# Optimization experiments

Measured on AMD Instinct MI355X. Metric: run time of the kernel, lower is better.

Reference implementation:

```python
import jax, jax.numpy as jnp
import numpy as np

B, S, D = 4, 2048, 1024
E = 8           # num_experts
TOP_K = 2
H = 3 * D       # hidden_mult = 3


def setup_inputs() -> dict:
    key = jax.random.key(0)
    ks = jax.random.split(key, 5)
    scale_d = 1.0 / np.sqrt(D)
    scale_h = 1.0 / np.sqrt(H)
    return {
        "x": jax.random.normal(ks[0], (B, S, D), dtype=jnp.float32),
        "gate_w": jax.random.normal(ks[1], (D, E), dtype=jnp.float32) * scale_d,
        "w1": jax.random.normal(ks[2], (E, D, H), dtype=jnp.float32) * scale_d,
        "w3": jax.random.normal(ks[3], (E, D, H), dtype=jnp.float32) * scale_d,
        "w2": jax.random.normal(ks[4], (E, H, D), dtype=jnp.float32) * scale_h,
    }


def reference(x, gate_w, w1, w2, w3):
    b, s, d = x.shape
    t = b * s
    xf = x.reshape(t, d)                                  # [T, D]
    probs = jax.nn.softmax(xf @ gate_w, axis=-1)          # [T, E]
    vals, idx = jax.lax.top_k(probs, TOP_K)               # [T, K]
    w = vals / jnp.sum(vals, axis=-1, keepdims=True)      # renormalized top-k weights
    # per-token combine weight for each expert (scatter top-k weights)
    comb = jnp.zeros((t, E), dtype=x.dtype).at[
        jnp.arange(t)[:, None], idx
    ].add(w)                                              # [T, E]
    out = jnp.zeros_like(xf)
    for e in range(E):  # small fixed expert count
        h = jax.nn.silu(xf @ w1[e]) * (xf @ w3[e])        # [T, H] SwiGLU
        out = out + comb[:, e:e + 1] * (h @ w2[e])        # weighted combine
    return out.reshape(b, s, d)
```

## Files before the change

### kernel.cpp

```cpp
#include <hip/hip_runtime.h>
#include <stdint.h>

#define T_TOK 8192
#define DDIM 1024
#define NEXP 8
#define HDIM 3072

typedef __attribute__((ext_vector_type(8))) short bfrag;
typedef __attribute__((ext_vector_type(4))) float facc;

__device__ __forceinline__ void gload16(const void* g, void* l) {
  __builtin_amdgcn_global_load_lds(
      (const __attribute__((address_space(1))) void*)g,
      (__attribute__((address_space(3))) void*)l, 16, 0, 0);
}

__device__ __forceinline__ unsigned short f2bf(float f) {
  unsigned int u = __float_as_uint(f);
  u += 0x7FFFu + ((u >> 16) & 1u);
  return (unsigned short)(u >> 16);
}

__global__ __launch_bounds__(64) void gate_topk(
    const float* __restrict__ x, const float* __restrict__ gw,
    int* __restrict__ counts, int* __restrict__ tok_list,
    float* __restrict__ wt_list)
{
  const int t = blockIdx.x;
  const int lane = threadIdx.x;
  const float* xr = x + (size_t)t * DDIM;
  float p[NEXP];
#pragma unroll
  for (int e = 0; e < NEXP; ++e) p[e] = 0.f;
#pragma unroll 4
  for (int i = 0; i < DDIM / 64; ++i) {
    const int d = i * 64 + lane;
    const float xv = xr[d];
    const float4 g0 = *(const float4*)(gw + (size_t)d * NEXP);
    const float4 g1 = *(const float4*)(gw + (size_t)d * NEXP + 4);
    p[0] += xv * g0.x; p[1] += xv * g0.y; p[2] += xv * g0.z; p[3] += xv * g0.w;
    p[4] += xv * g1.x; p[5] += xv * g1.y; p[6] += xv * g1.z; p[7] += xv * g1.w;
  }
#pragma unroll
  for (int off = 32; off > 0; off >>= 1) {
#pragma unroll
    for (int e = 0; e < NEXP; ++e) p[e] += __shfl_down(p[e], off);
  }
  if (lane == 0) {
    int i1 = 0; float v1 = p[0];
#pragma unroll
    for (int e = 1; e < NEXP; ++e) if (p[e] > v1) { v1 = p[e]; i1 = e; }
    int i2 = -1; float v2 = -3.4e38f;
#pragma unroll
    for (int e = 0; e < NEXP; ++e) if (e != i1 && p[e] > v2) { v2 = p[e]; i2 = e; }
    const float w0 = 1.f / (1.f + __expf(v2 - v1));
    int q1 = atomicAdd(&counts[i1 * 32], 1);
    tok_list[i1 * T_TOK + q1] = t;
    wt_list[i1 * T_TOK + q1] = w0;
    int q2 = atomicAdd(&counts[i2 * 32], 1);
    tok_list[i2 * T_TOK + q2] = t;
    wt_list[i2 * T_TOK + q2] = 1.f - w0;
  }
}

__global__ void calc_offs(const int* __restrict__ counts, int* __restrict__ offs) {
  if (threadIdx.x == 0 && blockIdx.x == 0) {
    int a = 0;
#pragma unroll
    for (int e = 0; e < NEXP; ++e) { offs[e] = a; a += counts[e * 32]; }
    offs[NEXP] = a;
  }
}

__global__ __launch_bounds__(256) void convert_x(
    const float* __restrict__ x, unsigned short* __restrict__ xb)
{
  const size_t i8 = ((size_t)blockIdx.x * 256 + threadIdx.x) * 8;
  const float4 a = *(const float4*)(x + i8);
  const float4 b = *(const float4*)(x + i8 + 4);
  union { unsigned short s[8]; uint4 v; } t;
  t.s[0] = f2bf(a.x); t.s[1] = f2bf(a.y); t.s[2] = f2bf(a.z); t.s[3] = f2bf(a.w);
  t.s[4] = f2bf(b.x); t.s[5] = f2bf(b.y); t.s[6] = f2bf(b.z); t.s[7] = f2bf(b.w);
  *(uint4*)(xb + i8) = t.v;
}

__global__ __launch_bounds__(256) void convert_wT(
    const float* __restrict__ src, unsigned short* __restrict__ dst,
    int K, int N)
{
  const int e = blockIdx.z;
  const int k0 = blockIdx.x * 64;
  const int n0 = blockIdx.y * 128;
  const float* se = src + (size_t)e * K * N;
  unsigned short* de = dst + (size_t)e * N * K;
  __shared__ unsigned short Tb[64][130];
  const int tid = threadIdx.x;
#pragma unroll
  for (int i = 0; i < 8; ++i) {
    const int f = i * 256 + tid;
    const int kl = f >> 5, nq = (f & 31) * 4;
    const float4 v = *(const float4*)(se + (size_t)(k0 + kl) * N + n0 + nq);
    Tb[kl][nq + 0] = f2bf(v.x);
    Tb[kl][nq + 1] = f2bf(v.y);
    Tb[kl][nq + 2] = f2bf(v.z);
    Tb[kl][nq + 3] = f2bf(v.w);
  }
  __syncthreads();
#pragma unroll
  for (int i = 0; i < 4; ++i) {
    const int idx = i * 256 + tid;
    const int n = idx >> 3, up = idx & 7;
    const int kb = (up ^ (n & 7)) * 8;
    union { unsigned short s[8]; uint4 v; } t;
#pragma unroll
    for (int j = 0; j < 8; ++j) t.s[j] = Tb[kb + j][n];
    *(uint4*)(de + ((size_t)(n0 + n) * K + k0 + up * 8)) = t.v;
  }
}

__global__ __launch_bounds__(256, 2) void moe_gemm1(
    const unsigned short* __restrict__ xb, const unsigned short* __restrict__ w1t,
    const unsigned short* __restrict__ w3t, const int* __restrict__ counts,
    const int* __restrict__ offs, const int* __restrict__ tok_list,
    unsigned short* __restrict__ h_buf)
{
  const int e = blockIdx.z;
  const int cnt = counts[e * 32];
  const int p0 = blockIdx.y * 128;
  if (p0 >= cnt) return;
  const int n0 = blockIdx.x * 64;
  const int hbase = offs[e];

  __shared__ __align__(16) unsigned short As[128 * 64];
  __shared__ __align__(16) unsigned short B1s[64 * 64];
  __shared__ __align__(16) unsigned short B3s[64 * 64];

  const int tid = threadIdx.x;
  const int lane = tid & 63;
  const int wv = tid >> 6;
  const int wm = wv >> 1;
  const int wn = wv & 1;
  const int lr = lane & 15;
  const int lg = lane >> 4;
  const int l8 = lane >> 3;
  const int lu = lane & 7;
  const int aswz = (lu ^ l8) * 16;

  const int* tl = tok_list + e * T_TOK;

  const unsigned short* asrc[4];
#pragma unroll
  for (int i = 0; i < 4; ++i) {
    const int p = p0 + wv * 32 + i * 8 + l8;
    const int tok = (p < cnt) ? tl[p] : 0;
    asrc[i] = xb + (size_t)tok * DDIM;
  }
  const unsigned short* b1src[2];
  const unsigned short* b3src[2];
#pragma unroll
  for (int i = 0; i < 2; ++i) {
    const int n = n0 + wv * 16 + i * 8 + l8;
    b1src[i] = w1t + (size_t)(e * HDIM + n) * DDIM;
    b3src[i] = w3t + (size_t)(e * HDIM + n) * DDIM;
  }

  facc acc1[4][2], acc3[4][2];
#pragma unroll
  for (int m = 0; m < 4; ++m)
#pragma unroll
    for (int n = 0; n < 2; ++n)
#pragma unroll
      for (int q = 0; q < 4; ++q) { acc1[m][n][q] = 0.f; acc3[m][n][q] = 0.f; }

#pragma unroll 1
  for (int k0 = 0; k0 < DDIM; k0 += 64) {
#pragma unroll
    for (int i = 0; i < 4; ++i)
      gload16((const char*)asrc[i] + k0 * 2 + aswz, &As[(wv * 4 + i) * 512]);
#pragma unroll
    for (int i = 0; i < 2; ++i) {
      gload16((const char*)b1src[i] + k0 * 2 + lu * 16, &B1s[(wv * 2 + i) * 512]);
      gload16((const char*)b3src[i] + k0 * 2 + lu * 16, &B3s[(wv * 2 + i) * 512]);
    }
    __syncthreads();
#pragma unroll
    for (int ks = 0; ks < 2; ++ks) {
      bfrag a[4];
#pragma unroll
      for (int m = 0; m < 4; ++m) {
        const int r = wm * 64 + m * 16 + lr;
        const int u = (ks * 4 + lg) ^ (r & 7);
        a[m] = *(const bfrag*)&As[r * 64 + u * 8];
      }
#pragma unroll
      for (int n = 0; n < 2; ++n) {
        const int rb = wn * 32 + n * 16 + lr;
        const int u = (ks * 4 + lg) ^ (rb & 7);
        const bfrag b1 = *(const bfrag*)&B1s[rb * 64 + u * 8];
#pragma unroll
        for (int m = 0; m < 4; ++m)
          acc1[m][n] = __builtin_amdgcn_mfma_f32_16x16x32_bf16(a[m], b1, acc1[m][n], 0, 0, 0);
        const bfrag b3 = *(const bfrag*)&B3s[rb * 64 + u * 8];
#pragma unroll
        for (int m = 0; m < 4; ++m)
          acc3[m][n] = __builtin_amdgcn_mfma_f32_16x16x32_bf16(a[m], b3, acc3[m][n], 0, 0, 0);
      }
    }
    __syncthreads();
  }

#pragma unroll
  for (int m = 0; m < 4; ++m)
#pragma unroll
    for (int n = 0; n < 2; ++n)
#pragma unroll
      for (int q = 0; q < 4; ++q) {
        const float a1 = acc1[m][n][q];
        const float a3 = acc3[m][n][q];
        const float hv = a1 * a3 / (1.f + __expf(-a1));
        const int row = wm * 64 + m * 16 + lg * 4 + q;
        const int col = wn * 32 + n * 16 + lr;
        As[row * 64 + col] = f2bf(hv);
      }
  __syncthreads();
#pragma unroll
  for (int i = 0; i < 4; ++i) {
    const int idx = i * 256 + tid;
    const int r = idx >> 3, u = idx & 7;
    if (p0 + r < cnt)
      *(uint4*)(h_buf + ((size_t)(hbase + p0 + r) * HDIM + n0 + u * 8)) =
          *(const uint4*)&As[r * 64 + u * 8];
  }
}

__global__ __launch_bounds__(256, 2) void moe_gemm2(
    const unsigned short* __restrict__ h_buf, const unsigned short* __restrict__ w2t,
    const int* __restrict__ counts, const int* __restrict__ offs,
    const int* __restrict__ tok_list, const float* __restrict__ wt_list,
    float* __restrict__ out)
{
  const int e = blockIdx.z;
  const int cnt = counts[e * 32];
  const int p0 = blockIdx.y * 128;
  if (p0 >= cnt) return;
  const int n0 = blockIdx.x * 128;
  const int hbase = offs[e];

  __shared__ __align__(16) unsigned short Ah[128 * 64];
  __shared__ __align__(16) unsigned short Bw[128 * 64];

  const int tid = threadIdx.x;
  const int lane = tid & 63;
  const int wv = tid >> 6;
  const int wm = wv >> 1;
  const int wn = wv & 1;
  const int lr = lane & 15;
  const int lg = lane >> 4;
  const int l8 = lane >> 3;
  const int lu = lane & 7;
  const int aswz = (lu ^ l8) * 16;

  const int* tl = tok_list + e * T_TOK;
  const float* wl = wt_list + e * T_TOK;

  const unsigned short* asrc[4];
#pragma unroll
  for (int i = 0; i < 4; ++i) {
    const int p = p0 + wv * 32 + i * 8 + l8;
    const int hrow = hbase + ((p < cnt) ? p : 0);
    asrc[i] = h_buf + (size_t)hrow * HDIM;
  }
  const unsigned short* bsrc[4];
#pragma unroll
  for (int i = 0; i < 4; ++i) {
    const int n = n0 + wv * 32 + i * 8 + l8;
    bsrc[i] = w2t + (size_t)(e * DDIM + n) * HDIM;
  }

  facc acc[4][4];
#pragma unroll
  for (int m = 0; m < 4; ++m)
#pragma unroll
    for (int n = 0; n < 4; ++n)
#pragma unroll
      for (int q = 0; q < 4; ++q) acc[m][n][q] = 0.f;

#pragma unroll 1
  for (int k0 = 0; k0 < HDIM; k0 += 64) {
#pragma unroll
    for (int i = 0; i < 4; ++i)
      gload16((const char*)asrc[i] + k0 * 2 + aswz, &Ah[(wv * 4 + i) * 512]);
#pragma unroll
    for (int i = 0; i < 4; ++i)
      gload16((const char*)bsrc[i] + k0 * 2 + lu * 16, &Bw[(wv * 4 + i) * 512]);
    __syncthreads();
#pragma unroll
    for (int ks = 0; ks < 2; ++ks) {
      bfrag a[4];
#pragma unroll
      for (int m = 0; m < 4; ++m) {
        const int r = wm * 64 + m * 16 + lr;
        const int u = (ks * 4 + lg) ^ (r & 7);
        a[m] = *(const bfrag*)&Ah[r * 64 + u * 8];
      }
#pragma unroll
      for (int n = 0; n < 4; ++n) {
        const int rb = wn * 64 + n * 16 + lr;
        const int u = (ks * 4 + lg) ^ (rb & 7);
        const bfrag b = *(const bfrag*)&Bw[rb * 64 + u * 8];
#pragma unroll
        for (int m = 0; m < 4; ++m)
          acc[m][n] = __builtin_amdgcn_mfma_f32_16x16x32_bf16(a[m], b, acc[m][n], 0, 0, 0);
      }
    }
    __syncthreads();
  }

#pragma unroll
  for (int m = 0; m < 4; ++m)
#pragma unroll
    for (int q = 0; q < 4; ++q) {
      const int p = p0 + wm * 64 + m * 16 + lg * 4 + q;
      if (p < cnt) {
        const int tok = tl[p];
        const float wt = wl[p];
        float* dst = out + (size_t)tok * DDIM + n0 + wn * 64 + lr;
#pragma unroll
        for (int n = 0; n < 4; ++n)
          atomicAdd(dst + n * 16, acc[m][n][q] * wt);
      }
    }
}

__global__ __launch_bounds__(256) void moe_gemm1_fb(
    const float* __restrict__ x, const float* __restrict__ w1,
    const float* __restrict__ w3, const int* __restrict__ counts,
    const int* __restrict__ tok_list, unsigned short* __restrict__ h_buf,
    int e)
{
  const int cnt = counts[e * 32];
  const int p0 = blockIdx.y * 64;
  if (p0 >= cnt) return;
  const int n0 = blockIdx.x * 64;

  __shared__ unsigned short As[64][40];
  __shared__ unsigned short B1s[64][40];
  __shared__ unsigned short B3s[64][40];

  const int tid = threadIdx.x;
  const int lane = tid & 63;
  const int wv = tid >> 6;

  const float* w1e = w1 + (size_t)e * DDIM * HDIM;
  const float* w3e = w3 + (size_t)e * DDIM * HDIM;
  const int* tl = tok_list + e * T_TOK;

  const int arow = tid >> 2;
  const int akseg = (tid & 3) * 8;
  int tok = -1;
  if (p0 + arow < cnt) tok = tl[p0 + arow];

  const int bk = tid >> 3;
  const int bn4 = (tid & 7) * 4;

  facc acc1[4], acc3[4];
#pragma unroll
  for (int i = 0; i < 4; ++i)
#pragma unroll
    for (int j = 0; j < 4; ++j) { acc1[i][j] = 0.f; acc3[i][j] = 0.f; }

  const int mrow = wv * 16 + (lane & 15);
  const int kq = (lane >> 4) * 8;

  for (int k0 = 0; k0 < DDIM; k0 += 32) {
    {
      union { unsigned short s[8]; uint4 v; } tmp;
      if (tok >= 0) {
        const float* src = x + (size_t)tok * DDIM + k0 + akseg;
        const float4 f0 = *(const float4*)(src);
        const float4 f1 = *(const float4*)(src + 4);
        tmp.s[0]=f2bf(f0.x); tmp.s[1]=f2bf(f0.y); tmp.s[2]=f2bf(f0.z); tmp.s[3]=f2bf(f0.w);
        tmp.s[4]=f2bf(f1.x); tmp.s[5]=f2bf(f1.y); tmp.s[6]=f2bf(f1.z); tmp.s[7]=f2bf(f1.w);
      } else {
        tmp.v = make_uint4(0u, 0u, 0u, 0u);
      }
      *(uint4*)&As[arow][akseg] = tmp.v;
    }
#pragma unroll
    for (int pass = 0; pass < 2; ++pass) {
      const int n = bn4 + pass * 32;
      const float4 f1v = *(const float4*)(w1e + (size_t)(k0 + bk) * HDIM + n0 + n);
      B1s[n + 0][bk] = f2bf(f1v.x);
      B1s[n + 1][bk] = f2bf(f1v.y);
      B1s[n + 2][bk] = f2bf(f1v.z);
      B1s[n + 3][bk] = f2bf(f1v.w);
      const float4 f3v = *(const float4*)(w3e + (size_t)(k0 + bk) * HDIM + n0 + n);
      B3s[n + 0][bk] = f2bf(f3v.x);
      B3s[n + 1][bk] = f2bf(f3v.y);
      B3s[n + 2][bk] = f2bf(f3v.z);
      B3s[n + 3][bk] = f2bf(f3v.w);
    }
    __syncthreads();
    const bfrag a = *(const bfrag*)&As[mrow][kq];
#pragma unroll
    for (int nt = 0; nt < 4; ++nt) {
      const bfrag b1 = *(const bfrag*)&B1s[nt * 16 + (lane & 15)][kq];
      acc1[nt] = __builtin_amdgcn_mfma_f32_16x16x32_bf16(a, b1, acc1[nt], 0, 0, 0);
      const bfrag b3 = *(const bfrag*)&B3s[nt * 16 + (lane & 15)][kq];
      acc3[nt] = __builtin_amdgcn_mfma_f32_16x16x32_bf16(a, b3, acc3[nt], 0, 0, 0);
    }
    __syncthreads();
  }
  const int rbase = p0 + wv * 16 + ((lane >> 4) * 4);
  const int cbase = n0 + (lane & 15);
#pragma unroll
  for (int r = 0; r < 4; ++r) {
    const int p = rbase + r;
    if (p < cnt) {
      unsigned short* dst = h_buf + (size_t)p * HDIM + cbase;
#pragma unroll
      for (int nt = 0; nt < 4; ++nt) {
        const float a1 = acc1[nt][r];
        const float a3 = acc3[nt][r];
        const float hv = a1 * a3 / (1.f + __expf(-a1));
        dst[nt * 16] = f2bf(hv);
      }
    }
  }
}

__global__ __launch_bounds__(256) void moe_gemm2_fb(
    const unsigned short* __restrict__ h_buf, const float* __restrict__ w2,
    const int* __restrict__ counts, const int* __restrict__ tok_list,
    const float* __restrict__ wt_list, float* __restrict__ out, int e)
{
  const int cnt = counts[e * 32];
  const int p0 = blockIdx.y * 64;
  if (p0 >= cnt) return;
  const int n0 = blockIdx.x * 64;

  __shared__ unsigned short As[64][40];
  __shared__ unsigned short Bs[64][40];

  const int tid = threadIdx.x;
  const int lane = tid & 63;
  const int wv = tid >> 6;

  const float* w2e = w2 + (size_t)e * HDIM * DDIM;
  const int* tl = tok_list + e * T_TOK;
  const float* wl = wt_list + e * T_TOK;

  const int arow = tid >> 2;
  const int akseg = (tid & 3) * 8;
  const bool avalid = (p0 + arow < cnt);

  const int bk = tid >> 3;
  const int bn4 = (tid & 7) * 4;

  facc acc[4];
#pragma unroll
  for (int i = 0; i < 4; ++i)
#pragma unroll
    for (int j = 0; j < 4; ++j) acc[i][j] = 0.f;

  const int mrow = wv * 16 + (lane & 15);
  const int kq = (lane >> 4) * 8;

  for (int k0 = 0; k0 < HDIM; k0 += 32) {
    if (avalid) {
      *(uint4*)&As[arow][akseg] =
          *(const uint4*)(h_buf + (size_t)(p0 + arow) * HDIM + k0 + akseg);
    } else {
      *(uint4*)&As[arow][akseg] = make_uint4(0u, 0u, 0u, 0u);
    }
#pragma unroll
    for (int pass = 0; pass < 2; ++pass) {
      const int n = bn4 + pass * 32;
      const float4 f = *(const float4*)(w2e + (size_t)(k0 + bk) * DDIM + n0 + n);
      Bs[n + 0][bk] = f2bf(f.x);
      Bs[n + 1][bk] = f2bf(f.y);
      Bs[n + 2][bk] = f2bf(f.z);
      Bs[n + 3][bk] = f2bf(f.w);
    }
    __syncthreads();
    const bfrag a = *(const bfrag*)&As[mrow][kq];
#pragma unroll
    for (int nt = 0; nt < 4; ++nt) {
      const bfrag b = *(const bfrag*)&Bs[nt * 16 + (lane & 15)][kq];
      acc[nt] = __builtin_amdgcn_mfma_f32_16x16x32_bf16(a, b, acc[nt], 0, 0, 0);
    }
    __syncthreads();
  }
  const int rbase = p0 + wv * 16 + ((lane >> 4) * 4);
  const int cbase = n0 + (lane & 15);
#pragma unroll
  for (int r = 0; r < 4; ++r) {
    const int p = rbase + r;
    if (p < cnt) {
      const int tok = tl[p];
      const float wt = wl[p];
      float* dst = out + (size_t)tok * DDIM + cbase;
#pragma unroll
      for (int nt = 0; nt < 4; ++nt) {
        atomicAdd(dst + nt * 16, acc[nt][r] * wt);
      }
    }
  }
}

__global__ void ws_too_small(float* out, int n) {
  int i = blockIdx.x * 256 + threadIdx.x;
  if (i < n) out[i] = 1.0e6f;
}

extern "C" void kernel_launch(void* const* d_in, const int* in_sizes, int n_in,
                              void* d_out, int out_size, void* d_ws, size_t ws_size,
                              hipStream_t stream) {
  const float* x  = (const float*)d_in[0];
  const float* gw = (const float*)d_in[1];
  const float* w1 = (const float*)d_in[2];
  const float* w3 = (const float*)d_in[3];
  const float* w2 = (const float*)d_in[4];
  float* out = (float*)d_out;

  const size_t off_tok = 4096;
  const size_t off_wt  = off_tok + (size_t)NEXP * T_TOK * 4;
  const size_t off_xb  = off_wt + (size_t)NEXP * T_TOK * 4;
  const size_t off_w1t = off_xb + (size_t)T_TOK * DDIM * 2;
  const size_t off_w3t = off_w1t + (size_t)NEXP * DDIM * HDIM * 2;
  const size_t off_w2t = off_w3t + (size_t)NEXP * DDIM * HDIM * 2;
  const size_t off_h   = off_w2t + (size_t)NEXP * HDIM * DDIM * 2;
  const size_t need    = off_h + (size_t)(2 * T_TOK) * HDIM * 2;

  if (ws_size >= need) {
    int* counts = (int*)d_ws;
    int* offs = (int*)((char*)d_ws + 1024);
    int* tok_list = (int*)((char*)d_ws + off_tok);
    float* wt_list = (float*)((char*)d_ws + off_wt);
    unsigned short* xb  = (unsigned short*)((char*)d_ws + off_xb);
    unsigned short* w1t = (unsigned short*)((char*)d_ws + off_w1t);
    unsigned short* w3t = (unsigned short*)((char*)d_ws + off_w3t);
    unsigned short* w2t = (unsigned short*)((char*)d_ws + off_w2t);
    unsigned short* h_buf = (unsigned short*)((char*)d_ws + off_h);

    hipMemsetAsync(d_ws, 0, 4096, stream);
    hipMemsetAsync(out, 0, (size_t)out_size * sizeof(float), stream);

    convert_x<<<(T_TOK * DDIM) / (256 * 8), 256, 0, stream>>>(x, xb);
    convert_wT<<<dim3(DDIM / 64, HDIM / 128, NEXP), 256, 0, stream>>>(w1, w1t, DDIM, HDIM);
    convert_wT<<<dim3(DDIM / 64, HDIM / 128, NEXP), 256, 0, stream>>>(w3, w3t, DDIM, HDIM);
    convert_wT<<<dim3(HDIM / 64, DDIM / 128, NEXP), 256, 0, stream>>>(w2, w2t, HDIM, DDIM);
    gate_topk<<<T_TOK, 64, 0, stream>>>(x, gw, counts, tok_list, wt_list);
    calc_offs<<<1, 1, 0, stream>>>(counts, offs);
    moe_gemm1<<<dim3(HDIM / 64, T_TOK / 128, NEXP), 256, 0, stream>>>(
        xb, w1t, w3t, counts, offs, tok_list, h_buf);
    moe_gemm2<<<dim3(DDIM / 128, T_TOK / 128, NEXP), 256, 0, stream>>>(
        h_buf, w2t, counts, offs, tok_list, wt_list, out);
    return;
  }

  const size_t fb_off_tok = 1024;
  const size_t fb_off_wt  = fb_off_tok + (size_t)NEXP * T_TOK * 4;
  const size_t fb_off_h   = fb_off_wt + (size_t)NEXP * T_TOK * 4;
  const size_t fb_need    = fb_off_h + (size_t)T_TOK * HDIM * 2;
  if (ws_size < fb_need) {
    ws_too_small<<<(out_size + 255) / 256, 256, 0, stream>>>(out, out_size);
    return;
  }
  int* counts = (int*)d_ws;
  int* tok_list = (int*)((char*)d_ws + fb_off_tok);
  float* wt_list = (float*)((char*)d_ws + fb_off_wt);
  unsigned short* h_buf = (unsigned short*)((char*)d_ws + fb_off_h);

  hipMemsetAsync(counts, 0, 1024, stream);
  hipMemsetAsync(out, 0, (size_t)out_size * sizeof(float), stream);

  gate_topk<<<T_TOK, 64, 0, stream>>>(x, gw, counts, tok_list, wt_list);
  for (int e = 0; e < NEXP; ++e) {
    moe_gemm1_fb<<<dim3(HDIM / 64, T_TOK / 64), 256, 0, stream>>>(
        x, w1, w3, counts, tok_list, h_buf, e);
    moe_gemm2_fb<<<dim3(DDIM / 64, T_TOK / 64), 256, 0, stream>>>(
        h_buf, w2, counts, tok_list, wt_list, out, e);
  }
}
```

Measured before the change: 753.1 us.

## Widen MoE gemm1 N-tile and replace atomic scatter with partial buffer combine

The first expert GEMM now computes a 128-wide hidden tile per block instead of 64, doubling the accumulators and the B tiles in LDS so each gathered token row is reused across more columns. The second GEMM no longer scatters weighted results into the output with fp32 atomicAdd. It writes unweighted per-slot rows into a partial buffer that reuses the w1t/w3t workspace region. A new combine kernel uses per-token slot indices recorded by gate_topk to compute the weighted sum of the two expert rows, which also removes the output memset. The trade-offs are higher register pressure in gemm1, plus an extra 64MB partial write and read pass in place of atomic traffic.

Result: no change. 765.3 us (+1.6%).

```diff
diff --git a/kernel.cpp b/kernel.cpp
--- a/kernel.cpp
+++ b/kernel.cpp
@@ -24,7 +24,8 @@
 __global__ __launch_bounds__(64) void gate_topk(
     const float* __restrict__ x, const float* __restrict__ gw,
     int* __restrict__ counts, int* __restrict__ tok_list,
-    float* __restrict__ wt_list)
+    float* __restrict__ wt_list, int* __restrict__ slotA,
+    int* __restrict__ slotB)
 {
   const int t = blockIdx.x;
   const int lane = threadIdx.x;
@@ -57,9 +58,11 @@
     int q1 = atomicAdd(&counts[i1 * 32], 1);
     tok_list[i1 * T_TOK + q1] = t;
     wt_list[i1 * T_TOK + q1] = w0;
+    slotA[t] = i1 * T_TOK + q1;
     int q2 = atomicAdd(&counts[i2 * 32], 1);
     tok_list[i2 * T_TOK + q2] = t;
     wt_list[i2 * T_TOK + q2] = 1.f - w0;
+    slotB[t] = i2 * T_TOK + q2;
   }
 }
 
@@ -128,12 +131,13 @@
   const int cnt = counts[e * 32];
   const int p0 = blockIdx.y * 128;
   if (p0 >= cnt) return;
-  const int n0 = blockIdx.x * 64;
+  const int n0 = blockIdx.x * 128;
   const int hbase = offs[e];
 
-  __shared__ __align__(16) unsigned short As[128 * 64];
-  __shared__ __align__(16) unsigned short B1s[64 * 64];
-  __shared__ __align__(16) unsigned short B3s[64 * 64];
+  __shared__ __align__(16) unsigned short lds[24576];
+  unsigned short* As  = lds;
+  unsigned short* B1s = lds + 8192;
+  unsigned short* B3s = lds + 16384;
 
   const int tid = threadIdx.x;
   const int lane = tid & 63;
@@ -155,20 +159,20 @@
     const int tok = (p < cnt) ? tl[p] : 0;
     asrc[i] = xb + (size_t)tok * DDIM;
   }
-  const unsigned short* b1src[2];
-  const unsigned short* b3src[2];
-#pragma unroll
-  for (int i = 0; i < 2; ++i) {
-    const int n = n0 + wv * 16 + i * 8 + l8;
+  const unsigned short* b1src[4];
+  const unsigned short* b3src[4];
+#pragma unroll
+  for (int i = 0; i < 4; ++i) {
+    const int n = n0 + wv * 32 + i * 8 + l8;
     b1src[i] = w1t + (size_t)(e * HDIM + n) * DDIM;
     b3src[i] = w3t + (size_t)(e * HDIM + n) * DDIM;
   }
 
-  facc acc1[4][2], acc3[4][2];
+  facc acc1[4][4], acc3[4][4];
 #pragma unroll
   for (int m = 0; m < 4; ++m)
 #pragma unroll
-    for (int n = 0; n < 2; ++n)
+    for (int n = 0; n < 4; ++n)
 #pragma unroll
       for (int q = 0; q < 4; ++q) { acc1[m][n][q] = 0.f; acc3[m][n][q] = 0.f; }
 
@@ -178,10 +182,11 @@
     for (int i = 0; i < 4; ++i)
       gload16((const char*)asrc[i] + k0 * 2 + aswz, &As[(wv * 4 + i) * 512]);
 #pragma unroll
-    for (int i = 0; i < 2; ++i) {
-      gload16((const char*)b1src[i] + k0 * 2 + lu * 16, &B1s[(wv * 2 + i) * 512]);
-      gload16((const char*)b3src[i] + k0 * 2 + lu * 16, &B3s[(wv * 2 + i) * 512]);
-    }
+    for (int i = 0; i < 4; ++i)
+      gload16((const char*)b1src[i] + k0 * 2 + lu * 16, &B1s[(wv * 4 + i) * 512]);
+#pragma unroll
+    for (int i = 0; i < 4; ++i)
+      gload16((const char*)b3src[i] + k0 * 2 + lu * 16, &B3s[(wv * 4 + i) * 512]);
     __syncthreads();
 #pragma unroll
     for (int ks = 0; ks < 2; ++ks) {
@@ -193,8 +198,8 @@
         a[m] = *(const bfrag*)&As[r * 64 + u * 8];
       }
 #pragma unroll
-      for (int n = 0; n < 2; ++n) {
-        const int rb = wn * 32 + n * 16 + lr;
+      for (int n = 0; n < 4; ++n) {
+        const int rb = wn * 64 + n * 16 + lr;
         const int u = (ks * 4 + lg) ^ (rb & 7);
         const bfrag b1 = *(const bfrag*)&B1s[rb * 64 + u * 8];
 #pragma unroll
@@ -212,32 +217,31 @@
 #pragma unroll
   for (int m = 0; m < 4; ++m)
 #pragma unroll
-    for (int n = 0; n < 2; ++n)
+    for (int n = 0; n < 4; ++n)
 #pragma unroll
       for (int q = 0; q < 4; ++q) {
         const float a1 = acc1[m][n][q];
         const float a3 = acc3[m][n][q];
         const float hv = a1 * a3 / (1.f + __expf(-a1));
         const int row = wm * 64 + m * 16 + lg * 4 + q;
-        const int col = wn * 32 + n * 16 + lr;
-        As[row * 64 + col] = f2bf(hv);
+        const int col = wn * 64 + n * 16 + lr;
+        lds[row * 128 + col] = f2bf(hv);
       }
   __syncthreads();
 #pragma unroll
-  for (int i = 0; i < 4; ++i) {
+  for (int i = 0; i < 8; ++i) {
     const int idx = i * 256 + tid;
-    const int r = idx >> 3, u = idx & 7;
+    const int r = idx >> 4, u = idx & 15;
     if (p0 + r < cnt)
       *(uint4*)(h_buf + ((size_t)(hbase + p0 + r) * HDIM + n0 + u * 8)) =
-          *(const uint4*)&As[r * 64 + u * 8];
+          *(const uint4*)&lds[r * 128 + u * 8];
   }
 }
 
 __global__ __launch_bounds__(256, 2) void moe_gemm2(
     const unsigned short* __restrict__ h_buf, const unsigned short* __restrict__ w2t,
     const int* __restrict__ counts, const int* __restrict__ offs,
-    const int* __restrict__ tok_list, const float* __restrict__ wt_list,
-    float* __restrict__ out)
+    float* __restrict__ part)
 {
   const int e = blockIdx.z;
   const int cnt = counts[e * 32];
@@ -260,9 +264,6 @@
   const int lu = lane & 7;
   const int aswz = (lu ^ l8) * 16;
 
-  const int* tl = tok_list + e * T_TOK;
-  const float* wl = wt_list + e * T_TOK;
-
   const unsigned short* asrc[4];
 #pragma unroll
   for (int i = 0; i < 4; ++i) {
@@ -322,14 +323,78 @@
     for (int q = 0; q < 4; ++q) {
       const int p = p0 + wm * 64 + m * 16 + lg * 4 + q;
       if (p < cnt) {
-        const int tok = tl[p];
-        const float wt = wl[p];
-        float* dst = out + (size_t)tok * DDIM + n0 + wn * 64 + lr;
+        float* dst = part + (size_t)(hbase + p) * DDIM + n0 + wn * 64 + lr;
 #pragma unroll
         for (int n = 0; n < 4; ++n)
-          atomicAdd(dst + n * 16, acc[m][n][q] * wt);
-      }
-    }
+          dst[n * 16] = acc[m][n][q];
+      }
+    }
+}
+
+__global__ __launch_bounds__(256) void combine_out(
+    const float* __restrict__ part, const int* __restrict__ slotA,
+    const int* __restrict__ slotB, const float* __restrict__ wt_list,
+    const int* __restrict__ offs, float* __restrict__ out)
+{
+  const int t = blockIdx.x;
+  const int sA = slotA[t], sB = slotB[t];
+  const float wA = wt_list[sA], wB = wt_list[sB];
+  const int pA = offs[sA >> 13] + (sA & (T_TOK - 1));
+  const int pB = offs[sB >> 13] + (sB & (T_TOK - 1));
+  const float* ra = part + (size_t)pA * DDIM;
+  const float* rb = part + (size_t)pB * DDIM;
+  float* o = out + (size_t)t * DDIM;
+  const int i = threadIdx.x * 4;
+  const float4 a = *(const float4*)(ra + i);
+  const float4 b = *(const float4*)(rb + i);
+  float4 r;
+  r.x = wA * a.x + wB * b.x;
+  r.y = wA * a.y + wB * b.y;
+  r.z = wA * a.z + wB * b.z;
+  r.w = wA * a.w + wB * b.w;
+  *(float4*)(o + i) = r;
+}
+
+__global__ __launch_bounds__(64) void gate_topk_fb(
+    const float* __restrict__ x, const float* __restrict__ gw,
+    int* __restrict__ counts, int* __restrict__ tok_list,
+    float* __restrict__ wt_list)
+{
+  const int t = blockIdx.x;
+  const int lane = threadIdx.x;
+  const float* xr = x + (size_t)t * DDIM;
+  float p[NEXP];
+#pragma unroll
+  for (int e = 0; e < NEXP; ++e) p[e] = 0.f;
+#pragma unroll 4
+  for (int i = 0; i < DDIM / 64; ++i) {
+    const int d = i * 64 + lane;
+    const float xv = xr[d];
+    const float4 g0 = *(const float4*)(gw + (size_t)d * NEXP);
+    const float4 g1 = *(const float4*)(gw + (size_t)d * NEXP + 4);
+    p[0] += xv * g0.x; p[1] += xv * g0.y; p[2] += xv * g0.z; p[3] += xv * g0.w;
+    p[4] += xv * g1.x; p[5] += xv * g1.y; p[6] += xv * g1.z; p[7] += xv * g1.w;
+  }
+#pragma unroll
+  for (int off = 32; off > 0; off >>= 1) {
+#pragma unroll
+    for (int e = 0; e < NEXP; ++e) p[e] += __shfl_down(p[e], off);
+  }
+  if (lane == 0) {
+    int i1 = 0; float v1 = p[0];
+#pragma unroll
+    for (int e = 1; e < NEXP; ++e) if (p[e] > v1) { v1 = p[e]; i1 = e; }
+    int i2 = -1; float v2 = -3.4e38f;
+#pragma unroll
+    for (int e = 0; e < NEXP; ++e) if (e != i1 && p[e] > v2) { v2 = p[e]; i2 = e; }
+    const float w0 = 1.f / (1.f + __expf(v2 - v1));
+    int q1 = atomicAdd(&counts[i1 * 32], 1);
+    tok_list[i1 * T_TOK + q1] = t;
+    wt_list[i1 * T_TOK + q1] = w0;
+    int q2 = atomicAdd(&counts[i2 * 32], 1);
+    tok_list[i2 * T_TOK + q2] = t;
+    wt_list[i2 * T_TOK + q2] = 1.f - w0;
+  }
 }
 
 __global__ __launch_bounds__(256) void moe_gemm1_fb(
@@ -525,37 +590,43 @@
 
   const size_t off_tok = 4096;
   const size_t off_wt  = off_tok + (size_t)NEXP * T_TOK * 4;
-  const size_t off_xb  = off_wt + (size_t)NEXP * T_TOK * 4;
+  const size_t off_sA  = off_wt + (size_t)NEXP * T_TOK * 4;
+  const size_t off_sB  = off_sA + (size_t)T_TOK * 4;
+  const size_t off_xb  = off_sB + (size_t)T_TOK * 4;
   const size_t off_w1t = off_xb + (size_t)T_TOK * DDIM * 2;
   const size_t off_w3t = off_w1t + (size_t)NEXP * DDIM * HDIM * 2;
   const size_t off_w2t = off_w3t + (size_t)NEXP * DDIM * HDIM * 2;
   const size_t off_h   = off_w2t + (size_t)NEXP * HDIM * DDIM * 2;
   const size_t need    = off_h + (size_t)(2 * T_TOK) * HDIM * 2;
+  const size_t off_part = off_w1t;
 
   if (ws_size >= need) {
     int* counts = (int*)d_ws;
     int* offs = (int*)((char*)d_ws + 1024);
     int* tok_list = (int*)((char*)d_ws + off_tok);
     float* wt_list = (float*)((char*)d_ws + off_wt);
+    int* slotA = (int*)((char*)d_ws + off_sA);
+    int* slotB = (int*)((char*)d_ws + off_sB);
     unsigned short* xb  = (unsigned short*)((char*)d_ws + off_xb);
     unsigned short* w1t = (unsigned short*)((char*)d_ws + off_w1t);
     unsigned short* w3t = (unsigned short*)((char*)d_ws + off_w3t);
     unsigned short* w2t = (unsigned short*)((char*)d_ws + off_w2t);
     unsigned short* h_buf = (unsigned short*)((char*)d_ws + off_h);
+    float* part = (float*)((char*)d_ws + off_part);
 
     hipMemsetAsync(d_ws, 0, 4096, stream);
-    hipMemsetAsync(out, 0, (size_t)out_size * sizeof(float), stream);
 
     convert_x<<<(T_TOK * DDIM) / (256 * 8), 256, 0, stream>>>(x, xb);
     convert_wT<<<dim3(DDIM / 64, HDIM / 128, NEXP), 256, 0, stream>>>(w1, w1t, DDIM, HDIM);
     convert_wT<<<dim3(DDIM / 64, HDIM / 128, NEXP), 256, 0, stream>>>(w3, w3t, DDIM, HDIM);
     convert_wT<<<dim3(HDIM / 64, DDIM / 128, NEXP), 256, 0, stream>>>(w2, w2t, HDIM, DDIM);
-    gate_topk<<<T_TOK, 64, 0, stream>>>(x, gw, counts, tok_list, wt_list);
+    gate_topk<<<T_TOK, 64, 0, stream>>>(x, gw, counts, tok_list, wt_list, slotA, slotB);
     calc_offs<<<1, 1, 0, stream>>>(counts, offs);
-    moe_gemm1<<<dim3(HDIM / 64, T_TOK / 128, NEXP), 256, 0, stream>>>(
+    moe_gemm1<<<dim3(HDIM / 128, T_TOK / 128, NEXP), 256, 0, stream>>>(
         xb, w1t, w3t, counts, offs, tok_list, h_buf);
     moe_gemm2<<<dim3(DDIM / 128, T_TOK / 128, NEXP), 256, 0, stream>>>(
-        h_buf, w2t, counts, offs, tok_list, wt_list, out);
+        h_buf, w2t, counts, offs, part);
+    combine_out<<<T_TOK, 256, 0, stream>>>(part, slotA, slotB, wt_list, offs, out);
     return;
   }
 
@@ -575,7 +646,7 @@
   hipMemsetAsync(counts, 0, 1024, stream);
   hipMemsetAsync(out, 0, (size_t)out_size * sizeof(float), stream);
 
-  gate_topk<<<T_TOK, 64, 0, stream>>>(x, gw, counts, tok_list, wt_list);
+  gate_topk_fb<<<T_TOK, 64, 0, stream>>>(x, gw, counts, tok_list, wt_list);
   for (int e = 0; e < NEXP; ++e) {
     moe_gemm1_fb<<<dim3(HDIM / 64, T_TOK / 64), 256, 0, stream>>>(
         x, w1, w3, counts, tok_list, h_buf, e);
```
